# Performance work log

Hardware: AMD Instinct MI355X
Metric: run time of the kernel (lower is better)

Reference implementation:

```python
import jax, jax.numpy as jnp
import numpy as np
import math

N_HEADS = 16


def setup_inputs() -> dict:
    key = jax.random.key(0)
    ks = jax.random.split(key, 6)
    B, S, D = 2, 2048, 2048
    hd = D // N_HEADS  # 128
    scale = 0.02
    x = jax.random.normal(ks[0], (B, S, D), dtype=jnp.float32)
    wq = jax.random.normal(ks[1], (D, D), dtype=jnp.float32) * scale
    wk = jax.random.normal(ks[2], (D, D), dtype=jnp.float32) * scale
    wv = jax.random.normal(ks[3], (D, D), dtype=jnp.float32) * scale
    wo = jax.random.normal(ks[4], (D, D), dtype=jnp.float32) * scale
    # Rotary frequencies: theta = 10000^(-2i/hd), angle[t, i] = t * theta_i
    inv_freq = 1.0 / (10000.0 ** (jnp.arange(0, hd, 2, dtype=jnp.float32) / hd))  # [hd//2]
    angles = jnp.arange(S, dtype=jnp.float32)[:, None] * inv_freq[None, :]  # [S, hd//2]
    freqs_cos = jnp.cos(angles)
    freqs_sin = jnp.sin(angles)
    # Causal additive mask [1,1,S,S]
    causal = jnp.tril(jnp.ones((S, S), dtype=bool))
    mask = jnp.where(causal, 0.0, -1e9).astype(jnp.float32)[None, None]
    return {"x": x, "wq": wq, "wk": wk, "wv": wv, "wo": wo,
            "freqs_cos": freqs_cos, "freqs_sin": freqs_sin, "mask": mask}


def _apply_rope(t, cos, sin):
    # t: [B,S,H,hd]; cos/sin: [S, hd//2]. Complex mult on (even, odd) pairs.
    B, S, H, hd = t.shape
    tr = t.reshape(B, S, H, hd // 2, 2)
    t0, t1 = tr[..., 0], tr[..., 1]
    c = cos[None, :, None, :]
    s = sin[None, :, None, :]
    o0 = t0 * c - t1 * s
    o1 = t0 * s + t1 * c
    return jnp.stack([o0, o1], axis=-1).reshape(B, S, H, hd)


def reference(x, wq, wk, wv, wo, freqs_cos, freqs_sin, mask):
    B, S, D = x.shape
    H = N_HEADS
    hd = D // H
    # Projections (torch Linear: y = x @ W^T)
    q = jnp.einsum('bsd,ed->bse', x, wq).reshape(B, S, H, hd)
    k = jnp.einsum('bsd,ed->bse', x, wk).reshape(B, S, H, hd)
    v = jnp.einsum('bsd,ed->bse', x, wv).reshape(B, S, H, hd)
    q = _apply_rope(q, freqs_cos, freqs_sin)
    k = _apply_rope(k, freqs_cos, freqs_sin)
    # Attention: scores [B,H,S,S]
    scores = jnp.einsum('bshd,bthd->bhst', q, k) / math.sqrt(hd)
    scores = scores + mask[:, :, :S, :S]
    attn = jax.nn.softmax(scores.astype(jnp.float32), axis=-1).astype(q.dtype)
    out = jnp.einsum('bhst,bthd->bshd', attn, v).reshape(B, S, D)
    return jnp.einsum('bsd,ed->bse', out, wo)
```

## Files before the change

### kernel.cpp

```cpp
#include <hip/hip_runtime.h>

typedef unsigned short u16;
typedef __attribute__((ext_vector_type(8))) short short8;
typedef __attribute__((ext_vector_type(4))) short short4s;
typedef __attribute__((ext_vector_type(4))) float f32x4;

__device__ __forceinline__ u16 f2b(float f) {
  union { float f; unsigned u; } c; c.f = f;
  unsigned u = c.u;
  unsigned r = (u + 0x7FFFu + ((u >> 16) & 1u)) >> 16;
  return (u16)r;
}
__device__ __forceinline__ float b2f(u16 h) {
  union { unsigned u; float f; } c; c.u = ((unsigned)h) << 16;
  return c.f;
}

__device__ __forceinline__ void gload16(const u16* g, u16* l) {
  __builtin_amdgcn_global_load_lds((const __attribute__((address_space(1))) void*)g,
                                   (__attribute__((address_space(3))) void*)l, 16, 0, 0);
}

__device__ __forceinline__ short4s tr16(const u16* p) {
  short4s d;
  asm volatile("ds_read_b64_tr_b16 %0, %1"
               : "=v"(d)
               : "v"((const __attribute__((address_space(3))) u16*)p));
  return d;
}

#define MFMA(a, b, c) __builtin_amdgcn_mfma_f32_16x16x32_bf16(a, b, c, 0, 0, 0)

__global__ __launch_bounds__(256) void cast_all(const float* __restrict__ x,
                                                const float* __restrict__ wq,
                                                const float* __restrict__ wk,
                                                const float* __restrict__ wv,
                                                const float* __restrict__ wo,
                                                u16* __restrict__ xb,
                                                u16* __restrict__ wqkv,
                                                u16* __restrict__ wob) {
  int i = blockIdx.x * 256 + threadIdx.x;
  const float4* s; u16* d; int off;
  if (i < 2097152)      { s = (const float4*)x;  d = xb;            off = i; }
  else if (i < 3145728) { s = (const float4*)wq; d = wqkv;          off = i - 2097152; }
  else if (i < 4194304) { s = (const float4*)wk; d = wqkv + 4194304; off = i - 3145728; }
  else if (i < 5242880) { s = (const float4*)wv; d = wqkv + 8388608; off = i - 4194304; }
  else                  { s = (const float4*)wo; d = wob;           off = i - 5242880; }
  float4 v = s[off];
  ushort4 r;
  r.x = f2b(v.x); r.y = f2b(v.y); r.z = f2b(v.z); r.w = f2b(v.w);
  *(ushort4*)(d + (size_t)off * 4) = r;
}

__global__ __launch_bounds__(256) void rope_k(u16* __restrict__ qkv,
                                              const float* __restrict__ fc,
                                              const float* __restrict__ fs) {
  int idx = blockIdx.x * 256 + threadIdx.x;
  int m = idx >> 8;
  int c = idx & 255;
  int s = m & 2047;
  int i0 = (c * 4) & 63;
  u16* p = qkv + (size_t)m * 6144 + 2048 + c * 8;
  short8 v = *(short8*)p;
  float4 cs = *(const float4*)(fc + (size_t)s * 64 + i0);
  float4 sn = *(const float4*)(fs + (size_t)s * 64 + i0);
  float cc[4] = {cs.x, cs.y, cs.z, cs.w};
  float ss[4] = {sn.x, sn.y, sn.z, sn.w};
#pragma unroll
  for (int t = 0; t < 4; ++t) {
    float x0 = b2f((u16)v[2 * t]);
    float x1 = b2f((u16)v[2 * t + 1]);
    float o0 = x0 * cc[t] - x1 * ss[t];
    float o1 = x0 * ss[t] + x1 * cc[t];
    v[2 * t]     = (short)f2b(o0);
    v[2 * t + 1] = (short)f2b(o1);
  }
  *(short8*)p = v;
}

template <int F32OUT>
__global__ __launch_bounds__(512, 4) void gemm_nt_2ph(const u16* __restrict__ Ag,
                                                      const u16* __restrict__ Bg,
                                                      void* __restrict__ Cp,
                                                      int M, int N, int K) {
  __shared__ __align__(16) u16 lds[24576];
  const int tid = threadIdx.x;
  const int l = tid & 63, w = tid >> 6;
  const int wm = w >> 2, wn = w & 3;
  const int ln = l & 15, lk = l >> 4;
  const int nbn = N >> 8;
  const int nwg = (M >> 7) * nbn;
  const int wg = ((blockIdx.x & 7) * (nwg >> 3)) + (blockIdx.x >> 3);
  const int row0 = (wg / nbn) << 7;
  const int col0 = (wg % nbn) << 8;
  const int T = K >> 5;

  const int r0s = tid >> 2;
  const int j0s = ((tid & 3) ^ ((r0s >> 1) & 3)) << 3;

#define STAGE_A(t)                                                                    \
  gload16(Ag + (size_t)(row0 + r0s) * K + (t) * 32 + j0s,                             \
          lds + ((t) & 1) * 4096 + tid * 8);
#define STAGE_B(t, h)                                                                 \
  gload16(Bg + (size_t)(col0 + (h) * 128 + r0s) * K + (t) * 32 + j0s,                 \
          lds + 8192 + ((t) & 1) * 8192 + (h) * 4096 + tid * 8);

  f32x4 acc[4][4];
#pragma unroll
  for (int m = 0; m < 4; ++m)
#pragma unroll
    for (int n = 0; n < 4; ++n) acc[m][n] = (f32x4){0.f, 0.f, 0.f, 0.f};

  const int cx = ((lk ^ ((ln >> 1) & 3)) << 3);

  STAGE_A(0); STAGE_B(0, 0); STAGE_B(0, 1);
  STAGE_A(1); STAGE_B(1, 0); STAGE_B(1, 1);
  asm volatile("s_waitcnt vmcnt(3)" ::: "memory");
  __builtin_amdgcn_s_barrier();

  for (int t = 0; t < T; ++t) {
    const u16* aB = lds + (t & 1) * 4096;
    const u16* bB = lds + 8192 + (t & 1) * 8192 + (wn >> 1) * 4096;
    short8 bf[4];
    short8 af[2];
#pragma unroll
    for (int q = 0; q < 2; ++q) {
      if (q == 0) {
#pragma unroll
        for (int n = 0; n < 4; ++n)
          bf[n] = *(const short8*)&bB[((wn & 1) * 64 + n * 16 + ln) * 32 + cx];
      }
#pragma unroll
      for (int m2 = 0; m2 < 2; ++m2)
        af[m2] = *(const short8*)&aB[(wm * 64 + (q * 2 + m2) * 16 + ln) * 32 + cx];
      if (q == 0) {
        if (t >= 1 && t + 1 < T) STAGE_A(t + 1);
      } else {
        if (t + 2 < T) {
          STAGE_B(t + 2, 0);
          STAGE_B(t + 2, 1);
          asm volatile("s_waitcnt vmcnt(2)" ::: "memory");
        } else if (t + 1 < T) {
          asm volatile("s_waitcnt vmcnt(0)" ::: "memory");
        }
      }
      __builtin_amdgcn_sched_barrier(0);
      __builtin_amdgcn_s_barrier();
      __builtin_amdgcn_sched_barrier(0);
      __builtin_amdgcn_s_setprio(1);
#pragma unroll
      for (int m2 = 0; m2 < 2; ++m2)
#pragma unroll
        for (int n = 0; n < 4; ++n)
          acc[q * 2 + m2][n] = MFMA(af[m2], bf[n], acc[q * 2 + m2][n]);
      __builtin_amdgcn_s_setprio(0);
      __builtin_amdgcn_sched_barrier(0);
      __builtin_amdgcn_s_barrier();
      __builtin_amdgcn_sched_barrier(0);
    }
  }

#pragma unroll
  for (int m = 0; m < 4; ++m) {
    int r0 = row0 + wm * 64 + m * 16 + lk * 4;
#pragma unroll
    for (int n = 0; n < 4; ++n) {
      int cc = col0 + wn * 64 + n * 16 + ln;
#pragma unroll
      for (int j = 0; j < 4; ++j) {
        float v = acc[m][n][j];
        if (F32OUT) ((float*)Cp)[(size_t)(r0 + j) * N + cc] = v;
        else        ((u16*)Cp)[(size_t)(r0 + j) * N + cc]   = f2b(v);
      }
    }
  }
#undef STAGE_A
#undef STAGE_B
}

__global__ __launch_bounds__(256) void attn_fwd(const u16* __restrict__ qkv,
                                                const float* __restrict__ fc,
                                                const float* __restrict__ fs,
                                                u16* __restrict__ out) {
  __shared__ __align__(16) u16 sK[2][64 * 128];
  __shared__ __align__(16) u16 sV[2][64 * 128];
  __shared__ __align__(16) u16 sP[4][16 * 72];
  const int tid = threadIdx.x, l = tid & 63, w = tid >> 6;
  const int ln = l & 15, lk = l >> 4;

  const int bid = blockIdx.x;
  const int l0 = ((bid & 7) << 6) + (bid >> 3);
  const int bh = l0 >> 4, pr = l0 & 15;
  const int b = bh >> 4, h = bh & 15;

  const u16* Kp = qkv + (size_t)b * 2048 * 6144 + 2048 + h * 128;
  const u16* Vp = Kp + 2048;
  const float scale = 0.08838834764831845f;

  for (int pass = 0; pass < 2; ++pass) {
    const int qt = pass ? (31 - pr) : pr;
    const int m0 = b * 2048 + qt * 64;
    const u16* Qp = qkv + (size_t)m0 * 6144 + h * 128;
    const int srow = qt * 64 + w * 16 + ln;

    short8 qf[4];
#pragma unroll
    for (int kc = 0; kc < 4; ++kc) {
      short8 raw = *(const short8*)(Qp + (size_t)(w * 16 + ln) * 6144 + kc * 32 + lk * 8);
      float4 c4 = *(const float4*)(fc + (size_t)srow * 64 + kc * 16 + lk * 4);
      float4 s4 = *(const float4*)(fs + (size_t)srow * 64 + kc * 16 + lk * 4);
      float cc[4] = {c4.x * scale, c4.y * scale, c4.z * scale, c4.w * scale};
      float ss[4] = {s4.x * scale, s4.y * scale, s4.z * scale, s4.w * scale};
#pragma unroll
      for (int t = 0; t < 4; ++t) {
        float x0 = b2f((u16)raw[2 * t]);
        float x1 = b2f((u16)raw[2 * t + 1]);
        qf[kc][2 * t]     = (short)f2b(x0 * cc[t] - x1 * ss[t]);
        qf[kc][2 * t + 1] = (short)f2b(x0 * ss[t] + x1 * cc[t]);
      }
    }

    f32x4 o[8];
#pragma unroll
    for (int d = 0; d < 8; ++d) o[d] = (f32x4){0.f, 0.f, 0.f, 0.f};
    float mrow[4] = {-1e9f, -1e9f, -1e9f, -1e9f};
    float lsum[4] = {0.f, 0.f, 0.f, 0.f};

    const int ntl = qt + 1;

    {
#pragma unroll
      for (int q = 0; q < 4; ++q) {
        int e = q * 256 + tid;
        int r = e >> 4, p = e & 15;
        gload16(Kp + (size_t)r * 6144 + ((p ^ (r & 7)) << 3), &sK[0][e * 8]);
        int j = ((e >> 6) << 2) + ((e & 7) >> 1);
        int d = (((e >> 3) & 7) << 4) + ((e & 1) << 3);
        gload16(Vp + (size_t)j * 6144 + d, &sV[0][e * 8]);
      }
    }
    __syncthreads();

    int cur = 0;
    for (int jt = 0; jt < ntl; ++jt) {
      if (jt + 1 < ntl) {
        const u16* Kt = Kp + (size_t)(jt + 1) * 64 * 6144;
        const u16* Vt = Vp + (size_t)(jt + 1) * 64 * 6144;
        int nb = cur ^ 1;
#pragma unroll
        for (int q = 0; q < 4; ++q) {
          int e = q * 256 + tid;
          int r = e >> 4, p = e & 15;
          gload16(Kt + (size_t)r * 6144 + ((p ^ (r & 7)) << 3), &sK[nb][e * 8]);
          int j = ((e >> 6) << 2) + ((e & 7) >> 1);
          int d = (((e >> 3) & 7) << 4) + ((e & 1) << 3);
          gload16(Vt + (size_t)j * 6144 + d, &sV[nb][e * 8]);
        }
      }

      f32x4 sf[4];
      __builtin_amdgcn_s_setprio(1);
#pragma unroll
      for (int nc = 0; nc < 4; ++nc) {
        f32x4 s = (f32x4){0.f, 0.f, 0.f, 0.f};
#pragma unroll
        for (int kc = 0; kc < 4; ++kc) {
          int r = nc * 16 + ln;
          short8 kb = *(const short8*)&sK[cur][r * 128 + (((kc << 2) + lk) ^ (r & 7)) * 8];
          s = MFMA(qf[kc], kb, s);
        }
        sf[nc] = s;
      }
      __builtin_amdgcn_s_setprio(0);

      if (jt == qt) {
        int ig = w * 16 + lk * 4;
#pragma unroll
        for (int nc = 0; nc < 4; ++nc) {
          int jg = nc * 16 + ln;
#pragma unroll
          for (int j = 0; j < 4; ++j)
            sf[nc][j] = (jg > ig + j) ? -1e9f : sf[nc][j];
        }
      }

      float tm[4];
#pragma unroll
      for (int j = 0; j < 4; ++j)
        tm[j] = fmaxf(fmaxf(sf[0][j], sf[1][j]), fmaxf(sf[2][j], sf[3][j]));
      int ok = (tm[0] <= mrow[0] + 8.f) & (tm[1] <= mrow[1] + 8.f) &
               (tm[2] <= mrow[2] + 8.f) & (tm[3] <= mrow[3] + 8.f);
      if (!__all(ok)) {
#pragma unroll
        for (int off = 1; off < 16; off <<= 1)
#pragma unroll
          for (int j = 0; j < 4; ++j) tm[j] = fmaxf(tm[j], __shfl_xor(tm[j], off, 16));
        float al[4];
#pragma unroll
        for (int j = 0; j < 4; ++j) {
          float nm = fmaxf(mrow[j], tm[j]);
          al[j] = __expf(mrow[j] - nm);
          mrow[j] = nm;
        }
#pragma unroll
        for (int d = 0; d < 8; ++d)
#pragma unroll
          for (int j = 0; j < 4; ++j) o[d][j] *= al[j];
#pragma unroll
        for (int j = 0; j < 4; ++j) lsum[j] *= al[j];
      }

#pragma unroll
      for (int nc = 0; nc < 4; ++nc)
#pragma unroll
        for (int j = 0; j < 4; ++j) {
          float p = __expf(sf[nc][j] - mrow[j]);
          u16 pb = f2b(p);
          sP[w][(lk * 4 + j) * 72 + nc * 16 + ln] = pb;
          lsum[j] += b2f(pb);
        }

      short8 pa0 = *(const short8*)&sP[w][ln * 72 + lk * 8];
      short8 pa1 = *(const short8*)&sP[w][ln * 72 + 32 + lk * 8];
      asm volatile("s_waitcnt lgkmcnt(0)" ::: "memory");
      __builtin_amdgcn_sched_barrier(0);

      short4s tb[4][4];
#define TRISSUE(dblk, slot)                                                  \
      {                                                                      \
        const u16* vb = &sV[cur][(lk * 2) * 512 + (dblk) * 64 + ln * 4];     \
        tb[slot][0] = tr16(vb);                                              \
        tb[slot][1] = tr16(vb + 512);                                        \
        tb[slot][2] = tr16(vb + 4096);                                       \
        tb[slot][3] = tr16(vb + 4096 + 512);                                 \
      }
      TRISSUE(0, 0);
      TRISSUE(1, 1);
      __builtin_amdgcn_s_setprio(1);
#pragma unroll
      for (int d = 0; d < 8; ++d) {
        if (d < 6) TRISSUE(d + 2, (d + 2) & 3);
        if (d < 6)       asm volatile("s_waitcnt lgkmcnt(8)" ::: "memory");
        else if (d == 6) asm volatile("s_waitcnt lgkmcnt(4)" ::: "memory");
        else             asm volatile("s_waitcnt lgkmcnt(0)" ::: "memory");
        __builtin_amdgcn_sched_barrier(0);
        short8 vb0 = {tb[d & 3][0][0], tb[d & 3][0][1], tb[d & 3][0][2], tb[d & 3][0][3],
                      tb[d & 3][1][0], tb[d & 3][1][1], tb[d & 3][1][2], tb[d & 3][1][3]};
        short8 vb1 = {tb[d & 3][2][0], tb[d & 3][2][1], tb[d & 3][2][2], tb[d & 3][2][3],
                      tb[d & 3][3][0], tb[d & 3][3][1], tb[d & 3][3][2], tb[d & 3][3][3]};
        o[d] = MFMA(pa0, vb0, o[d]);
        o[d] = MFMA(pa1, vb1, o[d]);
      }
      __builtin_amdgcn_s_setprio(0);
#undef TRISSUE

      __syncthreads();
      cur ^= 1;
    }

#pragma unroll
    for (int off = 1; off < 16; off <<= 1)
#pragma unroll
      for (int j = 0; j < 4; ++j) lsum[j] += __shfl_xor(lsum[j], off, 16);
    float inv[4];
#pragma unroll
    for (int j = 0; j < 4; ++j) inv[j] = 1.f / lsum[j];
#pragma unroll
    for (int d = 0; d < 8; ++d)
#pragma unroll
      for (int j = 0; j < 4; ++j)
        out[(size_t)(m0 + w * 16 + lk * 4 + j) * 2048 + h * 128 + d * 16 + ln] =
            f2b(o[d][j] * inv[j]);
  }
}

extern "C" void kernel_launch(void* const* d_in, const int* in_sizes, int n_in,
                              void* d_out, int out_size, void* d_ws, size_t ws_size,
                              hipStream_t stream) {
  const float* x  = (const float*)d_in[0];
  const float* wq = (const float*)d_in[1];
  const float* wk = (const float*)d_in[2];
  const float* wv = (const float*)d_in[3];
  const float* wo = (const float*)d_in[4];
  const float* fc = (const float*)d_in[5];
  const float* fs = (const float*)d_in[6];

  char* ws = (char*)d_ws;
  u16* xb   = (u16*)(ws);
  u16* wqkv = (u16*)(ws + 16777216);
  u16* wob  = (u16*)(ws + 41943040);
  u16* qkv  = (u16*)(ws + 50331648);
  u16* aout = (u16*)(ws + 100663296);

  cast_all<<<24576, 256, 0, stream>>>(x, wq, wk, wv, wo, xb, wqkv, wob);
  gemm_nt_2ph<0><<<768, 512, 0, stream>>>(xb, wqkv, qkv, 4096, 6144, 2048);
  rope_k<<<4096, 256, 0, stream>>>(qkv, fc, fs);
  attn_fwd<<<512, 256, 0, stream>>>(qkv, fc, fs, aout);
  gemm_nt_2ph<1><<<256, 512, 0, stream>>>(aout, wob, d_out, 4096, 2048, 2048);
}
```

Measured before the change: 279.5 us.

## Widen attention query tile to 128 rows and re-pipeline GEMM K-loop staging

The attention kernel now uses 512 threads (8 waves) per block, each block covering 128 query rows. Every staged K/V tile is therefore reused by twice as many query rows, and the grid shrinks to 256 blocks. The causal mask now applies to the last two key tiles using global indices. Separately, the GEMM main loop is manually split into two half-phases that issue the B loads earlier and the A loads after a barrier, with adjusted vmcnt waits. The goal is fewer K/V global loads and better overlap of loads with compute, at the cost of fewer blocks for load balance and higher per-block LDS and register pressure.

```diff
diff --git a/kernel.cpp b/kernel.cpp
--- a/kernel.cpp
+++ b/kernel.cpp
@@ -113,8 +113,8 @@
 
   const int cx = ((lk ^ ((ln >> 1) & 3)) << 3);
 
-  STAGE_A(0); STAGE_B(0, 0); STAGE_B(0, 1);
-  STAGE_A(1); STAGE_B(1, 0); STAGE_B(1, 1);
+  STAGE_B(0, 0); STAGE_B(0, 1); STAGE_A(0);
+  STAGE_B(1, 0); STAGE_B(1, 1); STAGE_A(1);
   asm volatile("s_waitcnt vmcnt(3)" ::: "memory");
   __builtin_amdgcn_s_barrier();
 
@@ -123,41 +123,48 @@
     const u16* bB = lds + 8192 + (t & 1) * 8192 + (wn >> 1) * 4096;
     short8 bf[4];
     short8 af[2];
-#pragma unroll
-    for (int q = 0; q < 2; ++q) {
-      if (q == 0) {
-#pragma unroll
-        for (int n = 0; n < 4; ++n)
-          bf[n] = *(const short8*)&bB[((wn & 1) * 64 + n * 16 + ln) * 32 + cx];
-      }
-#pragma unroll
-      for (int m2 = 0; m2 < 2; ++m2)
-        af[m2] = *(const short8*)&aB[(wm * 64 + (q * 2 + m2) * 16 + ln) * 32 + cx];
-      if (q == 0) {
-        if (t >= 1 && t + 1 < T) STAGE_A(t + 1);
-      } else {
-        if (t + 2 < T) {
-          STAGE_B(t + 2, 0);
-          STAGE_B(t + 2, 1);
-          asm volatile("s_waitcnt vmcnt(2)" ::: "memory");
-        } else if (t + 1 < T) {
-          asm volatile("s_waitcnt vmcnt(0)" ::: "memory");
-        }
-      }
-      __builtin_amdgcn_sched_barrier(0);
-      __builtin_amdgcn_s_barrier();
-      __builtin_amdgcn_sched_barrier(0);
-      __builtin_amdgcn_s_setprio(1);
-#pragma unroll
-      for (int m2 = 0; m2 < 2; ++m2)
-#pragma unroll
-        for (int n = 0; n < 4; ++n)
-          acc[q * 2 + m2][n] = MFMA(af[m2], bf[n], acc[q * 2 + m2][n]);
-      __builtin_amdgcn_s_setprio(0);
-      __builtin_amdgcn_sched_barrier(0);
-      __builtin_amdgcn_s_barrier();
-      __builtin_amdgcn_sched_barrier(0);
-    }
+
+#pragma unroll
+    for (int n = 0; n < 4; ++n)
+      bf[n] = *(const short8*)&bB[((wn & 1) * 64 + n * 16 + ln) * 32 + cx];
+#pragma unroll
+    for (int m2 = 0; m2 < 2; ++m2)
+      af[m2] = *(const short8*)&aB[(wm * 64 + m2 * 16 + ln) * 32 + cx];
+    __builtin_amdgcn_sched_barrier(0);
+    __builtin_amdgcn_s_barrier();
+    __builtin_amdgcn_sched_barrier(0);
+    __builtin_amdgcn_s_setprio(1);
+#pragma unroll
+    for (int m2 = 0; m2 < 2; ++m2)
+#pragma unroll
+      for (int n = 0; n < 4; ++n)
+        acc[m2][n] = MFMA(af[m2], bf[n], acc[m2][n]);
+    __builtin_amdgcn_s_setprio(0);
+    __builtin_amdgcn_sched_barrier(0);
+    __builtin_amdgcn_s_barrier();
+    __builtin_amdgcn_sched_barrier(0);
+
+#pragma unroll
+    for (int m2 = 0; m2 < 2; ++m2)
+      af[m2] = *(const short8*)&aB[(wm * 64 + (2 + m2) * 16 + ln) * 32 + cx];
+    if (t + 2 < T) { STAGE_B(t + 2, 0); STAGE_B(t + 2, 1); }
+    __builtin_amdgcn_sched_barrier(0);
+    __builtin_amdgcn_s_barrier();
+    __builtin_amdgcn_sched_barrier(0);
+    if (t + 2 < T) STAGE_A(t + 2);
+    __builtin_amdgcn_s_setprio(1);
+#pragma unroll
+    for (int m2 = 0; m2 < 2; ++m2)
+#pragma unroll
+      for (int n = 0; n < 4; ++n)
+        acc[2 + m2][n] = MFMA(af[m2], bf[n], acc[2 + m2][n]);
+    __builtin_amdgcn_s_setprio(0);
+    __builtin_amdgcn_sched_barrier(0);
+    if (t + 2 < T) { asm volatile("s_waitcnt vmcnt(3)" ::: "memory"); }
+    else           { asm volatile("s_waitcnt vmcnt(0)" ::: "memory"); }
+    __builtin_amdgcn_sched_barrier(0);
+    __builtin_amdgcn_s_barrier();
+    __builtin_amdgcn_sched_barrier(0);
   }
 
 #pragma unroll
@@ -178,19 +185,19 @@
 #undef STAGE_B
 }
 
-__global__ __launch_bounds__(256) void attn_fwd(const u16* __restrict__ qkv,
+__global__ __launch_bounds__(512) void attn_fwd(const u16* __restrict__ qkv,
                                                 const float* __restrict__ fc,
                                                 const float* __restrict__ fs,
                                                 u16* __restrict__ out) {
   __shared__ __align__(16) u16 sK[2][64 * 128];
   __shared__ __align__(16) u16 sV[2][64 * 128];
-  __shared__ __align__(16) u16 sP[4][16 * 72];
+  __shared__ __align__(16) u16 sP[8][16 * 72];
   const int tid = threadIdx.x, l = tid & 63, w = tid >> 6;
   const int ln = l & 15, lk = l >> 4;
 
   const int bid = blockIdx.x;
-  const int l0 = ((bid & 7) << 6) + (bid >> 3);
-  const int bh = l0 >> 4, pr = l0 & 15;
+  const int l0 = ((bid & 7) << 5) | (bid >> 3);
+  const int bh = l0 >> 3, pr = l0 & 7;
   const int b = bh >> 4, h = bh & 15;
 
   const u16* Kp = qkv + (size_t)b * 2048 * 6144 + 2048 + h * 128;
@@ -198,10 +205,10 @@
   const float scale = 0.08838834764831845f;
 
   for (int pass = 0; pass < 2; ++pass) {
-    const int qt = pass ? (31 - pr) : pr;
-    const int m0 = b * 2048 + qt * 64;
+    const int qt = pass ? (15 - pr) : pr;
+    const int m0 = b * 2048 + qt * 128;
     const u16* Qp = qkv + (size_t)m0 * 6144 + h * 128;
-    const int srow = qt * 64 + w * 16 + ln;
+    const int srow = qt * 128 + w * 16 + ln;
 
     short8 qf[4];
 #pragma unroll
@@ -226,12 +233,12 @@
     float mrow[4] = {-1e9f, -1e9f, -1e9f, -1e9f};
     float lsum[4] = {0.f, 0.f, 0.f, 0.f};
 
-    const int ntl = qt + 1;
+    const int ntl = 2 * qt + 2;
 
     {
 #pragma unroll
-      for (int q = 0; q < 4; ++q) {
-        int e = q * 256 + tid;
+      for (int q = 0; q < 2; ++q) {
+        int e = q * 512 + tid;
         int r = e >> 4, p = e & 15;
         gload16(Kp + (size_t)r * 6144 + ((p ^ (r & 7)) << 3), &sK[0][e * 8]);
         int j = ((e >> 6) << 2) + ((e & 7) >> 1);
@@ -248,8 +255,8 @@
         const u16* Vt = Vp + (size_t)(jt + 1) * 64 * 6144;
         int nb = cur ^ 1;
 #pragma unroll
-        for (int q = 0; q < 4; ++q) {
-          int e = q * 256 + tid;
+        for (int q = 0; q < 2; ++q) {
+          int e = q * 512 + tid;
           int r = e >> 4, p = e & 15;
           gload16(Kt + (size_t)r * 6144 + ((p ^ (r & 7)) << 3), &sK[nb][e * 8]);
           int j = ((e >> 6) << 2) + ((e & 7) >> 1);
@@ -273,11 +280,11 @@
       }
       __builtin_amdgcn_s_setprio(0);
 
-      if (jt == qt) {
-        int ig = w * 16 + lk * 4;
+      if (jt >= 2 * qt) {
+        int ig = qt * 128 + w * 16 + lk * 4;
 #pragma unroll
         for (int nc = 0; nc < 4; ++nc) {
-          int jg = nc * 16 + ln;
+          int jg = jt * 64 + nc * 16 + ln;
 #pragma unroll
           for (int j = 0; j < 4; ++j)
             sf[nc][j] = (jg > ig + j) ? -1e9f : sf[nc][j];
@@ -395,6 +402,6 @@
   cast_all<<<24576, 256, 0, stream>>>(x, wq, wk, wv, wo, xb, wqkv, wob);
   gemm_nt_2ph<0><<<768, 512, 0, stream>>>(xb, wqkv, qkv, 4096, 6144, 2048);
   rope_k<<<4096, 256, 0, stream>>>(qkv, fc, fs);
-  attn_fwd<<<512, 256, 0, stream>>>(qkv, fc, fs, aout);
+  attn_fwd<<<256, 512, 0, stream>>>(qkv, fc, fs, aout);
   gemm_nt_2ph<1><<<256, 512, 0, stream>>>(aout, wob, d_out, 4096, 2048, 2048);
 }
```

New measurement: 270.3 us. 3.3% less time.
